# Kernel optimization log

Hardware: AMD Instinct MI355X
Metric: run time of the kernel (lower is better)

Reference implementation:

```python
import jax, jax.numpy as jnp
import numpy as np

B, LQ, LKV = 4, 512, 4096
IN_DIM, N_HEADS, DIM_HEAD = 1024, 16, 64
INNER = N_HEADS * DIM_HEAD


def setup_inputs() -> dict:
    key = jax.random.key(0)
    ks = jax.random.split(key, 6)
    q = jax.random.normal(ks[0], (B, LQ, IN_DIM), dtype=jnp.float32)
    kv = jax.random.normal(ks[1], (B, LKV, IN_DIM), dtype=jnp.float32)
    mask = jax.random.randint(ks[2], (B, 1, 1, LKV), 0, 2).astype(jnp.bool_)
    w_scale = 0.02
    Wq = jax.random.normal(ks[3], (IN_DIM, INNER), dtype=jnp.float32) * w_scale
    Wkv = jax.random.normal(ks[4], (IN_DIM, 2 * INNER), dtype=jnp.float32) * w_scale
    Wo = jax.random.normal(ks[5], (INNER, IN_DIM), dtype=jnp.float32) * w_scale
    return {"q": q, "kv": kv, "mask": mask, "Wq": Wq, "Wkv": Wkv, "Wo": Wo}


def reference(q, kv, mask, Wq, Wkv, Wo):
    # projections
    qp = q @ Wq                                  # [B, LQ, INNER]
    kvp = kv @ Wkv                               # [B, LKV, 2*INNER]
    # split heads
    qh = qp.reshape(B, LQ, N_HEADS, DIM_HEAD).transpose(0, 2, 1, 3)   # [B,H,LQ,D]
    kvh = kvp.reshape(B, LKV, N_HEADS, 2 * DIM_HEAD).transpose(0, 2, 1, 3)
    kh, vh = kvh[..., :DIM_HEAD], kvh[..., DIM_HEAD:]                 # [B,H,LKV,D]
    scale = jnp.sqrt(jnp.asarray(DIM_HEAD, dtype=qh.dtype))
    scores = jnp.einsum("bhqd,bhkd->bhqk", qh, kh) / scale            # [B,H,LQ,LKV]
    scores = jnp.where(mask, -jnp.inf, scores)
    weights = jax.nn.softmax(scores, axis=-1)
    context = jnp.einsum("bhqk,bhkd->bhqd", weights, vh)              # [B,H,LQ,D]
    context = context.transpose(0, 2, 1, 3).reshape(B, LQ, INNER)
    return context @ Wo                                               # [B,LQ,IN_DIM]
```

## Files before the change

kernel.cpp:

```cpp
#include <hip/hip_runtime.h>
#include <hip/hip_bf16.h>
#include <math.h>

#define B_      4
#define LQ_     512
#define LKV_    4096
#define IN_DIM_ 1024
#define NH_     16
#define DH_     64
#define INNER_  1024

typedef _Float16 f16x8 __attribute__((ext_vector_type(8)));
typedef _Float16 f16x4 __attribute__((ext_vector_type(4)));
typedef float    f32x4 __attribute__((ext_vector_type(4)));

#define GLDS(gp, lp) __builtin_amdgcn_global_load_lds( \
    (const __attribute__((address_space(1))) void*)(gp), \
    (__attribute__((address_space(3))) void*)(lp), 16, 0, 0)

__global__ __launch_bounds__(256) void scan_mask(const int* __restrict__ mask,
                                                 int* __restrict__ pidx,
                                                 int* __restrict__ cnt) {
  __shared__ int wsum_s[4];
  int b = blockIdx.x, tid = threadIdx.x;
  const int* mb = mask + b * LKV_;
  int base = tid * 16;
  int vals[16];
#pragma unroll
  for (int i = 0; i < 4; ++i) {
    int4 v = *(const int4*)(mb + base + i * 4);
    vals[i * 4 + 0] = v.x; vals[i * 4 + 1] = v.y;
    vals[i * 4 + 2] = v.z; vals[i * 4 + 3] = v.w;
  }
  int s = 0;
#pragma unroll
  for (int j = 0; j < 16; ++j) s += (vals[j] == 0);
  int lane = tid & 63, wave = tid >> 6;
  int inc = s;
#pragma unroll
  for (int d = 1; d < 64; d <<= 1) {
    int v = __shfl_up(inc, d);
    if (lane >= d) inc += v;
  }
  if (lane == 63) wsum_s[wave] = inc;
  __syncthreads();
  int woff = 0;
#pragma unroll
  for (int w = 0; w < 4; ++w)
    if (w < wave) woff += wsum_s[w];
  if (tid == 255) cnt[b] = woff + inc;
  int run = woff + inc - s;
#pragma unroll
  for (int i = 0; i < 4; ++i) {
    int4 o;
    int* op = &o.x;
#pragma unroll
    for (int j = 0; j < 4; ++j) { op[j] = run; run += (vals[i * 4 + j] == 0); }
    *(int4*)(pidx + b * LKV_ + base + i * 4) = o;
  }
}

__device__ __forceinline__ void transpose_tile(const float* __restrict__ in,
                                               _Float16* __restrict__ out,
                                               int K, int N, int xb, int yb,
                                               float (*t)[33]) {
  int bn = xb * 32, bk = yb * 32;
  int tx = threadIdx.x & 31, ty = threadIdx.x >> 5;
#pragma unroll
  for (int i = 0; i < 4; ++i) {
    int r = ty + i * 8;
    t[r][tx] = in[(size_t)(bk + r) * N + bn + tx];
  }
  __syncthreads();
#pragma unroll
  for (int i = 0; i < 4; ++i) {
    int r = ty + i * 8;
    out[(size_t)(bn + r) * K + bk + tx] = (_Float16)t[tx][r];
  }
}

__global__ __launch_bounds__(256) void prep_compact(
    const float* __restrict__ kv, const float* __restrict__ q,
    const float* __restrict__ Wq, const float* __restrict__ Wkv,
    const float* __restrict__ Wo, const int* __restrict__ mask,
    const int* __restrict__ pidx,
    _Float16* __restrict__ kv16, _Float16* __restrict__ q16,
    _Float16* __restrict__ Wqt, _Float16* __restrict__ Wkvt,
    _Float16* __restrict__ Wot) {
  __shared__ float t[32][33];
  const int id = blockIdx.x, tid = threadIdx.x;
  if (id < 16384) {
    if (mask[id] != 0) return;
    int b = id >> 12;
    int dst = b * LKV_ + pidx[id];
    float4 v = ((const float4*)(kv + (size_t)id * IN_DIM_))[tid];
    f16x4 h = {(_Float16)v.x, (_Float16)v.y, (_Float16)v.z, (_Float16)v.w};
    ((f16x4*)(kv16 + (size_t)dst * IN_DIM_))[tid] = h;
  } else if (id < 18432) {
    int i = (id - 16384) * 256 + tid;
    float4 v = ((const float4*)q)[i];
    f16x4 h = {(_Float16)v.x, (_Float16)v.y, (_Float16)v.z, (_Float16)v.w};
    ((f16x4*)q16)[i] = h;
  } else if (id < 19456) {
    int l = id - 18432;
    transpose_tile(Wq, Wqt, 1024, 1024, l & 31, l >> 5, t);
  } else if (id < 21504) {
    int l = id - 19456;
    transpose_tile(Wkv, Wkvt, 1024, 2048, l & 63, l >> 6, t);
  } else {
    int l = id - 21504;
    transpose_tile(Wo, Wot, 1024, 1024, l & 31, l >> 5, t);
  }
}

__global__ __launch_bounds__(256, 4) void proj_f16(
    const _Float16* __restrict__ kv16, const _Float16* __restrict__ Wkvt,
    const _Float16* __restrict__ q16, const _Float16* __restrict__ Wqt,
    _Float16* __restrict__ qp16, _Float16* __restrict__ Kp,
    _Float16* __restrict__ Vt, const int* __restrict__ Cnt) {
  const int id = (blockIdx.x & 7) * 272 + (blockIdx.x >> 3);
  const bool is_kv = (id < 2048);
  int brow, bcol;
  const _Float16 *Ab, *Bb;
  if (is_kv) {
    bcol = (id & 15) * 128;
    brow = (id >> 4) * 128;
    if ((brow & 4095) >= Cnt[brow >> 12]) return;
    Ab = kv16 + (size_t)brow * 1024;
    Bb = Wkvt + (size_t)bcol * 1024;
  } else {
    int l = id - 2048;
    bcol = (l & 7) * 128;
    brow = (l >> 3) * 128;
    Ab = q16 + (size_t)brow * 1024;
    Bb = Wqt + (size_t)bcol * 1024;
  }
  __shared__ _Float16 As[128 * 64];
  __shared__ _Float16 Bs[128 * 64];
  const int tid = threadIdx.x;
  const int wave = tid >> 6, lane = tid & 63;
  const int quad = lane >> 4, l16 = lane & 15;
  const int wm = (wave & 1) * 64, wn = (wave >> 1) * 64;
  const int ro8 = lane >> 3, c8 = lane & 7;

  f32x4 acc[4][4];
#pragma unroll
  for (int i = 0; i < 4; ++i)
#pragma unroll
    for (int j = 0; j < 4; ++j) acc[i][j] = (f32x4){0.f, 0.f, 0.f, 0.f};

  for (int k0 = 0; k0 < 1024; k0 += 64) {
    __syncthreads();
#pragma unroll
    for (int i = 0; i < 4; ++i) {
      int rbase = wave * 32 + i * 8;
      int row = rbase + ro8;
      int g = c8 ^ (row & 7);
      GLDS(Ab + (size_t)row * 1024 + k0 + g * 8, &As[rbase * 64]);
      GLDS(Bb + (size_t)row * 1024 + k0 + g * 8, &Bs[rbase * 64]);
    }
    __syncthreads();
#pragma unroll
    for (int ks = 0; ks < 2; ++ks) {
      f16x8 af[4], bf[4];
      int c = ks * 4 + quad;
#pragma unroll
      for (int mt = 0; mt < 4; ++mt) {
        int r = wm + mt * 16 + l16;
        af[mt] = *(const f16x8*)&As[r * 64 + ((c ^ (r & 7)) * 8)];
        int rb = wn + mt * 16 + l16;
        bf[mt] = *(const f16x8*)&Bs[rb * 64 + ((c ^ (rb & 7)) * 8)];
      }
#pragma unroll
      for (int mt = 0; mt < 4; ++mt)
#pragma unroll
        for (int nt = 0; nt < 4; ++nt)
          acc[mt][nt] = __builtin_amdgcn_mfma_f32_16x16x32_f16(af[mt], bf[nt], acc[mt][nt], 0, 0, 0);
    }
  }

#pragma unroll
  for (int mt = 0; mt < 4; ++mt) {
    int row0 = brow + wm + mt * 16 + quad * 4;
#pragma unroll
    for (int nt = 0; nt < 4; ++nt) {
      int col = bcol + wn + nt * 16 + l16;
      f32x4 v = acc[mt][nt];
      if (is_kv) {
        int h = col >> 7, w64 = col & 63;
        if ((col & 127) < 64) {
#pragma unroll
          for (int r = 0; r < 4; ++r)
            Kp[(size_t)(row0 + r) * INNER_ + h * 64 + w64] = (_Float16)v[r];
        } else {
          int b = row0 >> 12, key = row0 & 4095;
          f16x4 pk = {(_Float16)v[0], (_Float16)v[1], (_Float16)v[2], (_Float16)v[3]};
          *(f16x4*)&Vt[((size_t)((b * NH_ + h) * DH_) + w64) * LKV_ + key] = pk;
        }
      } else {
#pragma unroll
        for (int r = 0; r < 4; ++r)
          qp16[(size_t)(row0 + r) * 1024 + col] = (_Float16)v[r];
      }
    }
  }
}

__global__ __launch_bounds__(256, 3) void attn_f16(
    const _Float16* __restrict__ qp, const _Float16* __restrict__ Kp,
    const _Float16* __restrict__ Vt, const int* __restrict__ cnt,
    float* __restrict__ opart, float* __restrict__ lpart) {
  const int idx = blockIdx.x;
  const int bh = idx & 63, qt = (idx >> 6) & 7, half = idx >> 9;
  const int b = bh >> 4, h = bh & 15;
  __shared__ _Float16 Ks[128 * 64];
  __shared__ _Float16 Vts[64 * 128];
  __shared__ _Float16 Pl[64][136];

  const int tid = threadIdx.x;
  const int wave = tid >> 6, lane = tid & 63;
  const int quad = lane >> 4, l16 = lane & 15;
  const int ro8 = lane >> 3, gch8 = (lane & 7) ^ (ro8 & 7);
  const int ro16 = lane >> 4, ch16 = lane & 15;

  const int qrow = b * LQ_ + qt * 64 + wave * 16 + l16;
  const _Float16* qpr = qp + (size_t)qrow * INNER_ + h * DH_;
  f16x8 qf[2];
  qf[0] = *(const f16x8*)(qpr + quad * 8);
  qf[1] = *(const f16x8*)(qpr + 32 + quad * 8);

  const int c_act = cnt[b];
  const int tiles = (c_act + 127) >> 7;
  const int htiles = (tiles + 1) >> 1;
  const int t0 = half * htiles;
  const int t1 = (half == 0) ? htiles : tiles;

  float l_run = 0.f;
  f32x4 oacc[4];
#pragma unroll
  for (int i = 0; i < 4; ++i) oacc[i] = (f32x4){0.f, 0.f, 0.f, 0.f};

  const _Float16* kb = Kp + (size_t)(b * LKV_) * INNER_ + h * DH_;
  const _Float16* vb = Vt + (size_t)((b * NH_ + h) * DH_) * LKV_;

  for (int t = t0; t < t1; ++t) {
    __syncthreads();
#pragma unroll
    for (int i = 0; i < 4; ++i) {
      int rbase = wave * 32 + i * 8;
      GLDS(kb + (size_t)(t * 128 + rbase + ro8) * INNER_ + gch8 * 8, &Ks[rbase * 64]);
    }
#pragma unroll
    for (int i = 0; i < 4; ++i) {
      int rbase = wave * 16 + i * 4;
      int row = rbase + ro16;
      int gch = ch16 ^ (row & 15);
      GLDS(vb + (size_t)row * LKV_ + t * 128 + gch * 8, &Vts[rbase * 128]);
    }
    __syncthreads();

    f32x4 sacc[8];
#pragma unroll
    for (int i = 0; i < 8; ++i) sacc[i] = (f32x4){0.f, 0.f, 0.f, 0.f};
#pragma unroll
    for (int ks = 0; ks < 2; ++ks) {
      int c = ks * 4 + quad;
#pragma unroll
      for (int mt = 0; mt < 8; ++mt) {
        int krow = mt * 16 + l16;
        f16x8 af = *(const f16x8*)&Ks[krow * 64 + ((c ^ (krow & 7)) * 8)];
        sacc[mt] = __builtin_amdgcn_mfma_f32_16x16x32_f16(af, qf[ks], sacc[mt], 0, 0, 0);
      }
    }
    const int lim = c_act - t * 128;
    float psloc = 0.f;
#pragma unroll
    for (int mt = 0; mt < 8; ++mt) {
      f16x4 pk;
#pragma unroll
      for (int r = 0; r < 4; ++r) {
        int key = mt * 16 + quad * 4 + r;
        float s = sacc[mt][r] * 0.125f;
        if (key >= lim) s = -1e30f;
        float p = __expf(s - 8.0f);
        psloc += p;
        pk[r] = (_Float16)p;
      }
      *(f16x4*)&Pl[wave * 16 + l16][mt * 16 + quad * 4] = pk;
    }
    psloc += __shfl_xor(psloc, 16);
    psloc += __shfl_xor(psloc, 32);
    l_run += psloc;
#pragma unroll
    for (int ks = 0; ks < 4; ++ks) {
      int c = ks * 4 + quad;
      f16x8 bf = *(const f16x8*)&Pl[wave * 16 + l16][ks * 32 + quad * 8];
#pragma unroll
      for (int mt = 0; mt < 4; ++mt) {
        int drow = mt * 16 + l16;
        f16x8 af = *(const f16x8*)&Vts[drow * 128 + ((c ^ (drow & 15)) * 8)];
        oacc[mt] = __builtin_amdgcn_mfma_f32_16x16x32_f16(af, bf, oacc[mt], 0, 0, 0);
      }
    }
  }

  float* ob = opart + ((size_t)(half * 2048 + qrow)) * INNER_ + h * DH_;
#pragma unroll
  for (int mt = 0; mt < 4; ++mt)
    *(f32x4*)(ob + mt * 16 + quad * 4) = oacc[mt];
  if (quad == 0) lpart[(size_t)(half * 2048 + qrow) * NH_ + h] = l_run;
}

__global__ __launch_bounds__(256) void attn_fin(const float* __restrict__ opart,
                                                const float* __restrict__ lpart,
                                                _Float16* __restrict__ ctx) {
  int row = blockIdx.x, t = threadIdx.x;
  int h = t >> 4;
  float l = lpart[(size_t)row * NH_ + h] + lpart[(size_t)(2048 + row) * NH_ + h];
  float inv = (l > 0.f) ? 1.f / l : 0.f;
  f32x4 a = *(const f32x4*)(opart + (size_t)row * INNER_ + t * 4);
  f32x4 c = *(const f32x4*)(opart + (size_t)(2048 + row) * INNER_ + t * 4);
  f16x4 o;
#pragma unroll
  for (int r = 0; r < 4; ++r) o[r] = (_Float16)((a[r] + c[r]) * inv);
  *(f16x4*)(ctx + (size_t)row * INNER_ + t * 4) = o;
}

__global__ __launch_bounds__(256, 2) void gemm_out(
    const _Float16* __restrict__ A, const _Float16* __restrict__ Bt,
    float* __restrict__ C) {
  const int brow = blockIdx.y * 64, bcol = blockIdx.x * 128;
  __shared__ _Float16 As[64 * 128];
  __shared__ _Float16 Bs[128 * 128];
  const int tid = threadIdx.x;
  const int wave = tid >> 6, lane = tid & 63;
  const int quad = lane >> 4, l16 = lane & 15;
  const int wm = (wave & 1) * 32, wn = (wave >> 1) * 64;
  const int r4 = lane >> 4, ch = lane & 15;

  f32x4 acc[2][4];
#pragma unroll
  for (int i = 0; i < 2; ++i)
#pragma unroll
    for (int j = 0; j < 4; ++j) acc[i][j] = (f32x4){0.f, 0.f, 0.f, 0.f};

  const _Float16* Ab = A + (size_t)brow * 1024;
  const _Float16* Bb = Bt + (size_t)bcol * 1024;

  for (int k0 = 0; k0 < 1024; k0 += 128) {
    __syncthreads();
#pragma unroll
    for (int i = 0; i < 4; ++i) {
      int rbase = wave * 16 + i * 4;
      int row = rbase + r4;
      int g = ch ^ (row & 15);
      GLDS(Ab + (size_t)row * 1024 + k0 + g * 8, &As[rbase * 128]);
    }
#pragma unroll
    for (int i = 0; i < 8; ++i) {
      int rbase = wave * 32 + i * 4;
      int row = rbase + r4;
      int g = ch ^ (row & 15);
      GLDS(Bb + (size_t)row * 1024 + k0 + g * 8, &Bs[rbase * 128]);
    }
    __syncthreads();
#pragma unroll
    for (int ks = 0; ks < 4; ++ks) {
      f16x8 af[2], bf[4];
      int c = ks * 4 + quad;
#pragma unroll
      for (int mt = 0; mt < 2; ++mt) {
        int r = wm + mt * 16 + l16;
        af[mt] = *(const f16x8*)&As[r * 128 + ((c ^ (r & 15)) * 8)];
      }
#pragma unroll
      for (int nt = 0; nt < 4; ++nt) {
        int rb = wn + nt * 16 + l16;
        bf[nt] = *(const f16x8*)&Bs[rb * 128 + ((c ^ (rb & 15)) * 8)];
      }
#pragma unroll
      for (int mt = 0; mt < 2; ++mt)
#pragma unroll
        for (int nt = 0; nt < 4; ++nt)
          acc[mt][nt] = __builtin_amdgcn_mfma_f32_16x16x32_f16(af[mt], bf[nt], acc[mt][nt], 0, 0, 0);
    }
  }

#pragma unroll
  for (int mt = 0; mt < 2; ++mt) {
    int row0 = brow + wm + mt * 16 + quad * 4;
#pragma unroll
    for (int nt = 0; nt < 4; ++nt) {
      int col = bcol + wn + nt * 16 + l16;
      f32x4 v = acc[mt][nt];
#pragma unroll
      for (int r = 0; r < 4; ++r) C[(size_t)(row0 + r) * 1024 + col] = v[r];
    }
  }
}

extern "C" void kernel_launch(void* const* d_in, const int* in_sizes, int n_in,
                              void* d_out, int out_size, void* d_ws, size_t ws_size,
                              hipStream_t stream) {
  const float* q   = (const float*)d_in[0];
  const float* kv  = (const float*)d_in[1];
  const int* mask  = (const int*)d_in[2];
  const float* Wq  = (const float*)d_in[3];
  const float* Wkv = (const float*)d_in[4];
  const float* Wo  = (const float*)d_in[5];
  float* out = (float*)d_out;

  _Float16* p = (_Float16*)d_ws;
  _Float16* q16   = p; p += (size_t)2048 * 1024;
  _Float16* kv16  = p; p += (size_t)16384 * 1024;
  _Float16* Wqt   = p; p += (size_t)1024 * 1024;
  _Float16* Wkvt  = p; p += (size_t)2048 * 1024;
  _Float16* Wot   = p; p += (size_t)1024 * 1024;
  _Float16* qp16  = p; p += (size_t)2048 * 1024;
  _Float16* Kp    = p; p += (size_t)16384 * 1024;
  _Float16* Vt    = p; p += (size_t)16384 * 1024;
  _Float16* ctx16 = p; p += (size_t)2048 * 1024;
  float* opart = (float*)p; p += (size_t)2 * 4096 * 1024;
  float* lpart = (float*)p; p += (size_t)2 * 2048 * NH_ * 2;
  int* pidx = (int*)p;
  int* cnt  = pidx + 16384;

  scan_mask<<<4, 256, 0, stream>>>(mask, pidx, cnt);
  prep_compact<<<22528, 256, 0, stream>>>(kv, q, Wq, Wkv, Wo, mask, pidx,
                                          kv16, q16, Wqt, Wkvt, Wot);
  proj_f16<<<2176, 256, 0, stream>>>(kv16, Wkvt, q16, Wqt, qp16, Kp, Vt, cnt);
  attn_f16<<<1024, 256, 0, stream>>>(qp16, Kp, Vt, cnt, opart, lpart);
  attn_fin<<<2048, 256, 0, stream>>>(opart, lpart, ctx16);
  gemm_out<<<dim3(8, 32), 256, 0, stream>>>(ctx16, Wot, out);
}
```

Before: 258.2 us.

## Double-buffer LDS tiles in projection and output GEMMs to overlap loads with MFMA

Both the projection GEMM and the output GEMM now use two LDS buffers per operand. The next K tile is issued via global_load_lds while MFMAs run on the current tile, and one barrier per iteration replaces the previous two. The output GEMM's K tile shrinks from 128 to 64 and occupancy hints change (proj 4→2 blocks, gemm_out 2→3) to fit the extra LDS. The intent is to hide global load latency, at the cost of more LDS per block and lower occupancy in proj. Correctness relies on the hardware waitcnt before the barrier covering the async LDS loads.

Measured after the change: 294.3 us. +14.0%, slower.

```diff
diff --git a/kernel.cpp b/kernel.cpp
--- a/kernel.cpp
+++ b/kernel.cpp
@@ -113,7 +113,7 @@
   }
 }
 
-__global__ __launch_bounds__(256, 4) void proj_f16(
+__global__ __launch_bounds__(256, 2) void proj_f16(
     const _Float16* __restrict__ kv16, const _Float16* __restrict__ Wkvt,
     const _Float16* __restrict__ q16, const _Float16* __restrict__ Wqt,
     _Float16* __restrict__ qp16, _Float16* __restrict__ Kp,
@@ -135,8 +135,8 @@
     Ab = q16 + (size_t)brow * 1024;
     Bb = Wqt + (size_t)bcol * 1024;
   }
-  __shared__ _Float16 As[128 * 64];
-  __shared__ _Float16 Bs[128 * 64];
+  __shared__ _Float16 As[2][128 * 64];
+  __shared__ _Float16 Bs[2][128 * 64];
   const int tid = threadIdx.x;
   const int wave = tid >> 6, lane = tid & 63;
   const int quad = lane >> 4, l16 = lane & 15;
@@ -149,17 +149,17 @@
 #pragma unroll
     for (int j = 0; j < 4; ++j) acc[i][j] = (f32x4){0.f, 0.f, 0.f, 0.f};
 
-  for (int k0 = 0; k0 < 1024; k0 += 64) {
-    __syncthreads();
+  auto stage = [&](int p, int k0) {
 #pragma unroll
     for (int i = 0; i < 4; ++i) {
       int rbase = wave * 32 + i * 8;
       int row = rbase + ro8;
       int g = c8 ^ (row & 7);
-      GLDS(Ab + (size_t)row * 1024 + k0 + g * 8, &As[rbase * 64]);
-      GLDS(Bb + (size_t)row * 1024 + k0 + g * 8, &Bs[rbase * 64]);
-    }
-    __syncthreads();
+      GLDS(Ab + (size_t)row * 1024 + k0 + g * 8, &As[p][rbase * 64]);
+      GLDS(Bb + (size_t)row * 1024 + k0 + g * 8, &Bs[p][rbase * 64]);
+    }
+  };
+  auto compute = [&](int p) {
 #pragma unroll
     for (int ks = 0; ks < 2; ++ks) {
       f16x8 af[4], bf[4];
@@ -167,9 +167,9 @@
 #pragma unroll
       for (int mt = 0; mt < 4; ++mt) {
         int r = wm + mt * 16 + l16;
-        af[mt] = *(const f16x8*)&As[r * 64 + ((c ^ (r & 7)) * 8)];
+        af[mt] = *(const f16x8*)&As[p][r * 64 + ((c ^ (r & 7)) * 8)];
         int rb = wn + mt * 16 + l16;
-        bf[mt] = *(const f16x8*)&Bs[rb * 64 + ((c ^ (rb & 7)) * 8)];
+        bf[mt] = *(const f16x8*)&Bs[p][rb * 64 + ((c ^ (rb & 7)) * 8)];
       }
 #pragma unroll
       for (int mt = 0; mt < 4; ++mt)
@@ -177,7 +177,18 @@
         for (int nt = 0; nt < 4; ++nt)
           acc[mt][nt] = __builtin_amdgcn_mfma_f32_16x16x32_f16(af[mt], bf[nt], acc[mt][nt], 0, 0, 0);
     }
-  }
+  };
+
+  stage(0, 0);
+  __syncthreads();
+#pragma unroll
+  for (int t = 0; t < 15; ++t) {
+    const int cur = t & 1;
+    stage(cur ^ 1, (t + 1) * 64);
+    compute(cur);
+    __syncthreads();
+  }
+  compute(1);
 
 #pragma unroll
   for (int mt = 0; mt < 4; ++mt) {
@@ -326,17 +337,17 @@
   *(f16x4*)(ctx + (size_t)row * INNER_ + t * 4) = o;
 }
 
-__global__ __launch_bounds__(256, 2) void gemm_out(
+__global__ __launch_bounds__(256, 3) void gemm_out(
     const _Float16* __restrict__ A, const _Float16* __restrict__ Bt,
     float* __restrict__ C) {
   const int brow = blockIdx.y * 64, bcol = blockIdx.x * 128;
-  __shared__ _Float16 As[64 * 128];
-  __shared__ _Float16 Bs[128 * 128];
+  __shared__ _Float16 As[2][64 * 64];
+  __shared__ _Float16 Bs[2][128 * 64];
   const int tid = threadIdx.x;
   const int wave = tid >> 6, lane = tid & 63;
   const int quad = lane >> 4, l16 = lane & 15;
   const int wm = (wave & 1) * 32, wn = (wave >> 1) * 64;
-  const int r4 = lane >> 4, ch = lane & 15;
+  const int ro8 = lane >> 3, c8 = lane & 7;
 
   f32x4 acc[2][4];
 #pragma unroll
@@ -347,36 +358,36 @@
   const _Float16* Ab = A + (size_t)brow * 1024;
   const _Float16* Bb = Bt + (size_t)bcol * 1024;
 
-  for (int k0 = 0; k0 < 1024; k0 += 128) {
-    __syncthreads();
+  auto stage = [&](int p, int k0) {
+#pragma unroll
+    for (int i = 0; i < 2; ++i) {
+      int rbase = wave * 16 + i * 8;
+      int row = rbase + ro8;
+      int g = c8 ^ (row & 7);
+      GLDS(Ab + (size_t)row * 1024 + k0 + g * 8, &As[p][rbase * 64]);
+    }
 #pragma unroll
     for (int i = 0; i < 4; ++i) {
-      int rbase = wave * 16 + i * 4;
-      int row = rbase + r4;
-      int g = ch ^ (row & 15);
-      GLDS(Ab + (size_t)row * 1024 + k0 + g * 8, &As[rbase * 128]);
-    }
-#pragma unroll
-    for (int i = 0; i < 8; ++i) {
-      int rbase = wave * 32 + i * 4;
-      int row = rbase + r4;
-      int g = ch ^ (row & 15);
-      GLDS(Bb + (size_t)row * 1024 + k0 + g * 8, &Bs[rbase * 128]);
-    }
-    __syncthreads();
-#pragma unroll
-    for (int ks = 0; ks < 4; ++ks) {
+      int rbase = wave * 32 + i * 8;
+      int row = rbase + ro8;
+      int g = c8 ^ (row & 7);
+      GLDS(Bb + (size_t)row * 1024 + k0 + g * 8, &Bs[p][rbase * 64]);
+    }
+  };
+  auto compute = [&](int p) {
+#pragma unroll
+    for (int ks = 0; ks < 2; ++ks) {
       f16x8 af[2], bf[4];
       int c = ks * 4 + quad;
 #pragma unroll
       for (int mt = 0; mt < 2; ++mt) {
         int r = wm + mt * 16 + l16;
-        af[mt] = *(const f16x8*)&As[r * 128 + ((c ^ (r & 15)) * 8)];
+        af[mt] = *(const f16x8*)&As[p][r * 64 + ((c ^ (r & 7)) * 8)];
       }
 #pragma unroll
       for (int nt = 0; nt < 4; ++nt) {
         int rb = wn + nt * 16 + l16;
-        bf[nt] = *(const f16x8*)&Bs[rb * 128 + ((c ^ (rb & 15)) * 8)];
+        bf[nt] = *(const f16x8*)&Bs[p][rb * 64 + ((c ^ (rb & 7)) * 8)];
       }
 #pragma unroll
       for (int mt = 0; mt < 2; ++mt)
@@ -384,7 +395,18 @@
         for (int nt = 0; nt < 4; ++nt)
           acc[mt][nt] = __builtin_amdgcn_mfma_f32_16x16x32_f16(af[mt], bf[nt], acc[mt][nt], 0, 0, 0);
     }
-  }
+  };
+
+  stage(0, 0);
+  __syncthreads();
+#pragma unroll
+  for (int t = 0; t < 15; ++t) {
+    const int cur = t & 1;
+    stage(cur ^ 1, (t + 1) * 64);
+    compute(cur);
+    __syncthreads();
+  }
+  compute(1);
 
 #pragma unroll
   for (int mt = 0; mt < 2; ++mt) {
```
